# Optimization experiments

Hardware: AMD Instinct MI355X
Metric: run time of the kernel (lower is better)

## Reference

```python
import jax, jax.numpy as jnp
import numpy as np


def setup_inputs() -> dict:
    key = jax.random.key(0)
    k1, k2, k3 = jax.random.split(key, 3)
    N, K, H, W = 8, 8, 256, 256
    C, P = 32, 100000
    fragments = jax.random.randint(k1, (N, K, H, W), 0, P, dtype=jnp.int64)
    alphas = jax.random.uniform(k2, (N, K, H, W), dtype=jnp.float32)
    features = jax.random.normal(k3, (C, P), dtype=jnp.float32)
    return {"fragments": fragments, "alphas": alphas, "features": features}


def reference(fragments, alphas, features):
    # Alpha compositing (front-to-back over the K points-per-pixel axis):
    #   weight_k = alpha_k * prod_{j<k} (1 - alpha_j)
    #   out[n,c,h,w] = sum_k weight_k[n,k,h,w] * features[c, fragments[n,k,h,w]]
    # Indices < 0 mark empty fragment slots (sorted to the tail by the
    # rasterizer); treat them as alpha = 0 so they contribute nothing and
    # do not attenuate.
    valid = fragments >= 0                                   # (N,K,H,W)
    a = jnp.where(valid, alphas, 0.0)                        # (N,K,H,W)
    # exclusive cumulative product of transmittance (1 - alpha) along K
    trans = jnp.cumprod(1.0 - a, axis=1)                     # inclusive
    excl = jnp.concatenate(
        [jnp.ones_like(trans[:, :1]), trans[:, :-1]], axis=1
    )                                                        # exclusive
    weights = a * excl                                       # (N,K,H,W)
    idx = jnp.where(valid, fragments, 0)
    gathered = features[:, idx]                              # (C,N,K,H,W)
    images = jnp.einsum("cnkhw,nkhw->nchw", gathered, weights)
    return images
```

## Files before the change

kernel.cpp:

```cpp
#include <hip/hip_runtime.h>

#define N_IMG 8
#define K_LAY 8
#define C_CH  32
#define P_FEAT 100000
#define HW 65536
#define NPIX (N_IMG * HW)
#define NFEAT (C_CH * P_FEAT)

#define T_EPS 3e-3f

__global__ __launch_bounds__(256) void absmax_kernel(
    const float* __restrict__ f, unsigned int* __restrict__ out, int n)
{
    __shared__ float red[4];
    float m = 0.0f;
    for (int i = blockIdx.x * 256 + threadIdx.x; i < n; i += gridDim.x * 256)
        m = fmaxf(m, fabsf(f[i]));
    #pragma unroll
    for (int o = 32; o > 0; o >>= 1)
        m = fmaxf(m, __shfl_down(m, o, 64));
    if ((threadIdx.x & 63) == 0) red[threadIdx.x >> 6] = m;
    __syncthreads();
    if (threadIdx.x == 0) {
        m = fmaxf(fmaxf(red[0], red[1]), fmaxf(red[2], red[3]));
        atomicMax(out, __float_as_uint(m));
    }
}

__global__ __launch_bounds__(256) void transpose_feat_q(
    const float* __restrict__ feat, unsigned char* __restrict__ featQ,
    const unsigned int* __restrict__ maxbits)
{
    const float inv_s = 127.0f / __uint_as_float(*maxbits);
    __shared__ float tile[32][33];
    const int x  = threadIdx.x;
    const int y  = threadIdx.y;
    const int p0 = blockIdx.x * 32;

    #pragma unroll
    for (int j = 0; j < 4; ++j) {
        const int c = y * 4 + j;
        tile[c][x] = feat[(size_t)c * P_FEAT + p0 + x];
    }
    __syncthreads();

    const int t  = x + 32 * y;
    const int pl = t >> 3;
    const int c0 = (t & 7) * 4;
    union { unsigned char b[4]; unsigned int u; } pk;
    #pragma unroll
    for (int j = 0; j < 4; ++j) {
        const int q = (int)rintf(tile[c0 + j][pl] * inv_s);
        pk.b[j] = (unsigned char)(q + 127);
    }
    *reinterpret_cast<unsigned int*>(featQ + (size_t)(p0 + pl) * C_CH + c0) = pk.u;
}

__global__ __launch_bounds__(256) void composite(
    const int*           __restrict__ frag,
    const float*         __restrict__ alpha,
    const unsigned char* __restrict__ featQ,
    const unsigned int*  __restrict__ maxbits,
    float*               __restrict__ out)
{
    const float s = __uint_as_float(*maxbits) * (1.0f / 127.0f);

    const int tid = blockIdx.x * 256 + threadIdx.x;
    const int pix = tid >> 2;
    const int q   = tid & 3;
    const int n   = pix >> 16;
    const int p   = pix & (HW - 1);

    const int*   fb = frag  + (size_t)n * K_LAY * HW + p;
    const float* ab = alpha + (size_t)n * K_LAY * HW + p;

    int   f[K_LAY];
    float a[K_LAY];
    #pragma unroll
    for (int k = 0; k < K_LAY; ++k) f[k] = __builtin_nontemporal_load(fb + (size_t)k * HW);
    #pragma unroll
    for (int k = 0; k < K_LAY; ++k) a[k] = __builtin_nontemporal_load(ab + (size_t)k * HW);

    float w[K_LAY];
    int   idx[K_LAY];
    float T = 1.0f;
    #pragma unroll
    for (int k = 0; k < K_LAY; ++k) {
        const bool  valid = (f[k] >= 0);
        const float ak    = valid ? a[k] : 0.0f;
        const bool  live  = (T >= T_EPS) && valid;
        w[k]   = live ? ak * T * s : 0.0f;
        idx[k] = live ? f[k] : 0;
        T *= (1.0f - ak);
    }

    float acc[8];
    #pragma unroll
    for (int c = 0; c < 8; ++c) acc[c] = 0.0f;
    float Ws = 0.0f;

    #pragma unroll
    for (int k = 0; k < K_LAY; ++k) {
        const uint2 r = *reinterpret_cast<const uint2*>(
            featQ + (size_t)idx[k] * C_CH + q * 8);
        const float wk = w[k];
        Ws += wk;
        #pragma unroll
        for (int j = 0; j < 4; ++j)
            acc[j] = fmaf(wk, (float)((r.x >> (8 * j)) & 0xffu), acc[j]);
        #pragma unroll
        for (int j = 0; j < 4; ++j)
            acc[4 + j] = fmaf(wk, (float)((r.y >> (8 * j)) & 0xffu), acc[4 + j]);
    }

    const float bias = 127.0f * Ws;
    float* ob = out + ((size_t)n * C_CH + q * 8) * HW + p;
    #pragma unroll
    for (int j = 0; j < 8; ++j)
        __builtin_nontemporal_store(acc[j] - bias, ob + (size_t)j * HW);
}

__global__ __launch_bounds__(256) void composite_strided(
    const int*   __restrict__ frag,
    const float* __restrict__ alpha,
    const float* __restrict__ feat,
    float*       __restrict__ out)
{
    const int gid = blockIdx.x * 256 + threadIdx.x;
    const int n = gid >> 16;
    const int p = gid & (HW - 1);

    const int*   fb = frag  + (size_t)n * K_LAY * HW + p;
    const float* ab = alpha + (size_t)n * K_LAY * HW + p;

    float acc[C_CH];
    #pragma unroll
    for (int c = 0; c < C_CH; ++c) acc[c] = 0.0f;

    float T = 1.0f;
    #pragma unroll
    for (int k = 0; k < K_LAY; ++k) {
        if (T >= T_EPS) {
            const int   f = fb[(size_t)k * HW];
            float       a = ab[(size_t)k * HW];
            a = (f >= 0) ? a : 0.0f;
            const float wgt = a * T;
            T *= (1.0f - a);
            if (wgt > 0.0f) {
                #pragma unroll
                for (int c = 0; c < C_CH; ++c)
                    acc[c] = fmaf(wgt, feat[(size_t)c * P_FEAT + f], acc[c]);
            }
        }
    }

    float* ob = out + (size_t)n * C_CH * HW + p;
    #pragma unroll
    for (int c = 0; c < C_CH; ++c)
        ob[(size_t)c * HW] = acc[c];
}

extern "C" void kernel_launch(void* const* d_in, const int* in_sizes, int n_in,
                              void* d_out, int out_size, void* d_ws, size_t ws_size,
                              hipStream_t stream)
{
    const int*   frag  = (const int*)  d_in[0];
    const float* alpha = (const float*)d_in[1];
    const float* feat  = (const float*)d_in[2];
    float*       out   = (float*)d_out;

    const size_t need = 256 + (size_t)P_FEAT * C_CH;
    if (ws_size >= need) {
        unsigned int*  maxbits = (unsigned int*)d_ws;
        unsigned char* featQ   = (unsigned char*)d_ws + 256;

        hipMemsetAsync(maxbits, 0, 4, stream);
        absmax_kernel<<<dim3(512), dim3(256), 0, stream>>>(feat, maxbits, NFEAT);
        transpose_feat_q<<<dim3(P_FEAT / 32), dim3(32, 8), 0, stream>>>(feat, featQ, maxbits);
        composite<<<dim3((NPIX * 4) / 256), dim3(256), 0, stream>>>(frag, alpha, featQ, maxbits, out);
    } else {
        composite_strided<<<dim3(NPIX / 256), dim3(256), 0, stream>>>(frag, alpha, feat, out);
    }
}
```

Measured before the change: 160.4 us.

## Make composite persistent with register prefetch; vectorize absmax loads

The composite kernel now runs a fixed grid of 2048 blocks. Each thread loops over NCHUNK pixel chunks and prefetches the next chunk's fragment and alpha values into registers while it gathers and accumulates the current chunk. Output stores change from nontemporal to regular stores. The absmax reduction reads float4 and uses a larger grid. The prefetch doubles the live fragment and alpha registers and may lower occupancy, which matters for a latency-bound gather.

```diff
diff --git a/kernel.cpp b/kernel.cpp
--- a/kernel.cpp
+++ b/kernel.cpp
@@ -8,15 +8,22 @@
 #define NPIX (N_IMG * HW)
 #define NFEAT (C_CH * P_FEAT)
 
+#define CBLOCKS 2048
+#define CHUNK_PIX (CBLOCKS * 256 / 4)
+#define NCHUNK (NPIX / CHUNK_PIX)
+
 #define T_EPS 3e-3f
 
 __global__ __launch_bounds__(256) void absmax_kernel(
-    const float* __restrict__ f, unsigned int* __restrict__ out, int n)
+    const float4* __restrict__ f4, unsigned int* __restrict__ out, int n4)
 {
     __shared__ float red[4];
     float m = 0.0f;
-    for (int i = blockIdx.x * 256 + threadIdx.x; i < n; i += gridDim.x * 256)
-        m = fmaxf(m, fabsf(f[i]));
+    for (int i = blockIdx.x * 256 + threadIdx.x; i < n4; i += gridDim.x * 256) {
+        const float4 v = f4[i];
+        m = fmaxf(m, fmaxf(fmaxf(fabsf(v.x), fabsf(v.y)),
+                           fmaxf(fabsf(v.z), fabsf(v.w))));
+    }
     #pragma unroll
     for (int o = 32; o > 0; o >>= 1)
         m = fmaxf(m, __shfl_down(m, o, 64));
@@ -67,58 +74,83 @@
     const float s = __uint_as_float(*maxbits) * (1.0f / 127.0f);
 
     const int tid = blockIdx.x * 256 + threadIdx.x;
-    const int pix = tid >> 2;
     const int q   = tid & 3;
-    const int n   = pix >> 16;
-    const int p   = pix & (HW - 1);
-
-    const int*   fb = frag  + (size_t)n * K_LAY * HW + p;
-    const float* ab = alpha + (size_t)n * K_LAY * HW + p;
+    int pix = tid >> 2;
 
     int   f[K_LAY];
     float a[K_LAY];
-    #pragma unroll
-    for (int k = 0; k < K_LAY; ++k) f[k] = __builtin_nontemporal_load(fb + (size_t)k * HW);
-    #pragma unroll
-    for (int k = 0; k < K_LAY; ++k) a[k] = __builtin_nontemporal_load(ab + (size_t)k * HW);
-
-    float w[K_LAY];
-    int   idx[K_LAY];
-    float T = 1.0f;
-    #pragma unroll
-    for (int k = 0; k < K_LAY; ++k) {
-        const bool  valid = (f[k] >= 0);
-        const float ak    = valid ? a[k] : 0.0f;
-        const bool  live  = (T >= T_EPS) && valid;
-        w[k]   = live ? ak * T * s : 0.0f;
-        idx[k] = live ? f[k] : 0;
-        T *= (1.0f - ak);
-    }
-
-    float acc[8];
-    #pragma unroll
-    for (int c = 0; c < 8; ++c) acc[c] = 0.0f;
-    float Ws = 0.0f;
-
-    #pragma unroll
-    for (int k = 0; k < K_LAY; ++k) {
-        const uint2 r = *reinterpret_cast<const uint2*>(
-            featQ + (size_t)idx[k] * C_CH + q * 8);
-        const float wk = w[k];
-        Ws += wk;
-        #pragma unroll
-        for (int j = 0; j < 4; ++j)
-            acc[j] = fmaf(wk, (float)((r.x >> (8 * j)) & 0xffu), acc[j]);
-        #pragma unroll
-        for (int j = 0; j < 4; ++j)
-            acc[4 + j] = fmaf(wk, (float)((r.y >> (8 * j)) & 0xffu), acc[4 + j]);
-    }
-
-    const float bias = 127.0f * Ws;
-    float* ob = out + ((size_t)n * C_CH + q * 8) * HW + p;
-    #pragma unroll
-    for (int j = 0; j < 8; ++j)
-        __builtin_nontemporal_store(acc[j] - bias, ob + (size_t)j * HW);
+    {
+        const int n = pix >> 16, p = pix & (HW - 1);
+        const int*   fb = frag  + (size_t)n * K_LAY * HW + p;
+        const float* ab = alpha + (size_t)n * K_LAY * HW + p;
+        #pragma unroll
+        for (int k = 0; k < K_LAY; ++k)
+            f[k] = __builtin_nontemporal_load(fb + (size_t)k * HW);
+        #pragma unroll
+        for (int k = 0; k < K_LAY; ++k)
+            a[k] = __builtin_nontemporal_load(ab + (size_t)k * HW);
+    }
+
+    #pragma unroll
+    for (int it = 0; it < NCHUNK; ++it) {
+        int   nf[K_LAY];
+        float na[K_LAY];
+        const int npix = pix + CHUNK_PIX;
+        if (it < NCHUNK - 1) {
+            const int n2 = npix >> 16, p2 = npix & (HW - 1);
+            const int*   fb2 = frag  + (size_t)n2 * K_LAY * HW + p2;
+            const float* ab2 = alpha + (size_t)n2 * K_LAY * HW + p2;
+            #pragma unroll
+            for (int k = 0; k < K_LAY; ++k)
+                nf[k] = __builtin_nontemporal_load(fb2 + (size_t)k * HW);
+            #pragma unroll
+            for (int k = 0; k < K_LAY; ++k)
+                na[k] = __builtin_nontemporal_load(ab2 + (size_t)k * HW);
+        }
+
+        float w[K_LAY];
+        int   idx[K_LAY];
+        float T = 1.0f;
+        #pragma unroll
+        for (int k = 0; k < K_LAY; ++k) {
+            const bool  valid = (f[k] >= 0);
+            const float ak    = valid ? a[k] : 0.0f;
+            const bool  live  = (T >= T_EPS) && valid;
+            w[k]   = live ? ak * T * s : 0.0f;
+            idx[k] = live ? f[k] : 0;
+            T *= (1.0f - ak);
+        }
+
+        float acc[8];
+        #pragma unroll
+        for (int c = 0; c < 8; ++c) acc[c] = 0.0f;
+        float Ws = 0.0f;
+
+        #pragma unroll
+        for (int k = 0; k < K_LAY; ++k) {
+            const uint2 r = *reinterpret_cast<const uint2*>(
+                featQ + (size_t)idx[k] * C_CH + q * 8);
+            const float wk = w[k];
+            Ws += wk;
+            #pragma unroll
+            for (int j = 0; j < 4; ++j)
+                acc[j] = fmaf(wk, (float)((r.x >> (8 * j)) & 0xffu), acc[j]);
+            #pragma unroll
+            for (int j = 0; j < 4; ++j)
+                acc[4 + j] = fmaf(wk, (float)((r.y >> (8 * j)) & 0xffu), acc[4 + j]);
+        }
+
+        const float bias = 127.0f * Ws;
+        const int n = pix >> 16, p = pix & (HW - 1);
+        float* ob = out + ((size_t)n * C_CH + q * 8) * HW + p;
+        #pragma unroll
+        for (int j = 0; j < 8; ++j)
+            ob[(size_t)j * HW] = acc[j] - bias;
+
+        pix = npix;
+        #pragma unroll
+        for (int k = 0; k < K_LAY; ++k) { f[k] = nf[k]; a[k] = na[k]; }
+    }
 }
 
 __global__ __launch_bounds__(256) void composite_strided(
@@ -176,9 +208,10 @@
         unsigned char* featQ   = (unsigned char*)d_ws + 256;
 
         hipMemsetAsync(maxbits, 0, 4, stream);
-        absmax_kernel<<<dim3(512), dim3(256), 0, stream>>>(feat, maxbits, NFEAT);
+        absmax_kernel<<<dim3(2048), dim3(256), 0, stream>>>(
+            (const float4*)feat, maxbits, NFEAT / 4);
         transpose_feat_q<<<dim3(P_FEAT / 32), dim3(32, 8), 0, stream>>>(feat, featQ, maxbits);
-        composite<<<dim3((NPIX * 4) / 256), dim3(256), 0, stream>>>(frag, alpha, featQ, maxbits, out);
+        composite<<<dim3(CBLOCKS), dim3(256), 0, stream>>>(frag, alpha, featQ, maxbits, out);
     } else {
         composite_strided<<<dim3(NPIX / 256), dim3(256), 0, stream>>>(frag, alpha, feat, out);
     }
```

Result: slower. 167.3 us (+4.3%).
